# Optimization experiments

Measured on AMD Instinct MI355X. Metric: run time of the kernel, lower is better.

The kernel has to match this reference:

```python
import jax, jax.numpy as jnp
import numpy as np

MASK_FILL = -987654321.0


def rotate_every_two(x):
    # pairs (x0, x1) -> (-x1, x0), interleaved back along last dim
    x1 = x[..., 0::2]
    x2 = x[..., 1::2]
    return jnp.stack((-x2, x1), axis=-1).reshape(x.shape)


def setup_inputs() -> dict:
    key = jax.random.key(0)
    ks = jax.random.split(key, 6)
    b, n, dim = 64, 197, 768
    heads, dim_head = 12, 64
    inner = heads * dim_head
    x = jax.random.normal(ks[0], (b, n, dim), dtype=jnp.float32)
    pos_emb = jax.random.normal(ks[1], (1, n, dim_head), dtype=jnp.float32)
    w_qkv = jax.random.normal(ks[2], (dim, 3 * inner), dtype=jnp.float32) * (dim ** -0.5)
    scale = jnp.full((heads,), dim_head ** -0.5, dtype=jnp.float32)
    w_out = jax.random.normal(ks[3], (inner, dim), dtype=jnp.float32) * (inner ** -0.5)
    b_out = jnp.zeros((dim,), dtype=jnp.float32)
    return {"x": x, "pos_emb": pos_emb, "w_qkv": w_qkv, "scale": scale,
            "w_out": w_out, "b_out": b_out}


def reference(x, pos_emb, w_qkv, scale, w_out, b_out):
    b, n, dim = x.shape
    h = scale.shape[0]
    qkv = x @ w_qkv                         # [b, n, 3*inner]
    q, k, v = jnp.split(qkv, 3, axis=-1)
    dh = q.shape[-1] // h
    to_heads = lambda t: t.reshape(b, n, h, dh).transpose(0, 2, 1, 3)  # bhnd
    q, k, v = to_heads(q), to_heads(k), to_heads(v)

    # RoPE: pos_emb [1, n, (2 * dh/2)] -> sin/cos [n, dh/2] -> interleave to [n, dh]
    sc = pos_emb[0].reshape(n, 2, dh // 2)
    sin = jnp.repeat(sc[:, 0], 2, axis=-1)  # [n, dh]
    cos = jnp.repeat(sc[:, 1], 2, axis=-1)
    q = q * cos + rotate_every_two(q) * sin
    k = k * cos + rotate_every_two(k) * sin

    # per-head learnable scale
    dots = jnp.einsum('bhid,bhjd->bhij', q, k) * scale[None, :, None, None]
    # diagonal (LSA) mask
    eye = jnp.eye(n, dtype=bool)
    dots = jnp.where(eye, MASK_FILL, dots)

    attn = jax.nn.softmax(dots, axis=-1)
    out = jnp.einsum('bhij,bhjd->bhid', attn, v)
    out = out.transpose(0, 2, 1, 3).reshape(b, n, h * dh)
    return out @ w_out + b_out
```

## Files before the change

kernel.cpp:

```cpp
#include <hip/hip_runtime.h>
#include <math.h>

#define MASK_FILL_F (-987654321.0f)

typedef unsigned short u16;
typedef unsigned int   u32;

constexpr int Bb   = 64;
constexpr int Ntok = 197;
constexpr int Dim  = 768;
constexpr int Heads= 12;
constexpr int Dh   = 64;
constexpr int Nq3  = 2304;
constexpr int Rows = 12608;
constexpr int Mpad = 12672;

using f32x4  = __attribute__((ext_vector_type(4))) float;
using bf16x8 = __attribute__((ext_vector_type(8))) short;

__device__ __forceinline__ u16 f2bf(float f) {
  u32 u = __float_as_uint(f);
  u = (u + 0x7fffu + ((u >> 16) & 1u)) >> 16;
  return (u16)u;
}

__device__ __forceinline__ void stage16(const void* gp, void* lp) {
  __builtin_amdgcn_global_load_lds(
      (const __attribute__((address_space(1))) u32*)gp,
      (__attribute__((address_space(3))) u32*)lp, 16, 0, 0);
}

__device__ __forceinline__ int sigma6(int M) {
  return (M & 0x23) | (((M >> 3) & 1) << 4) | (((M >> 2) & 1) << 3) |
         (((M >> 4) & 1) << 2);
}

constexpr int NB_CVT = (Rows * Dim / 4 + 255) / 256;
constexpr int NB_TQ  = (Nq3 / 32) * (Dim / 32);
constexpr int NB_TO  = (Dim / 32) * (Dim / 32);

__global__ __launch_bounds__(256) void prep(
    const float* __restrict__ x, u16* __restrict__ xb,
    const float* __restrict__ w_qkv, u16* __restrict__ wqkvT,
    const float* __restrict__ w_out, u16* __restrict__ woutT)
{
  __shared__ float t[32][33];
  const int bid = blockIdx.x, tid = threadIdx.x;

  if (bid < NB_CVT) {
    const int i = bid * 256 + tid;
    if (i < Rows * Dim / 4) {
      const float4 v = *(const float4*)&x[(size_t)i * 4];
      ushort4 u;
      u.x = f2bf(v.x); u.y = f2bf(v.y); u.z = f2bf(v.z); u.w = f2bf(v.w);
      *(ushort4*)&xb[(size_t)i * 4] = u;
    }
    return;
  }

  const float* in; u16* out; int R, C, c0, r0;
  if (bid < NB_CVT + NB_TQ) {
    const int b2 = bid - NB_CVT;
    in = w_qkv; out = wqkvT; R = Dim; C = Nq3;
    c0 = (b2 % (Nq3 / 32)) * 32; r0 = (b2 / (Nq3 / 32)) * 32;
  } else {
    const int b3 = bid - NB_CVT - NB_TQ;
    in = w_out; out = woutT; R = Dim; C = Dim;
    c0 = (b3 % (Dim / 32)) * 32; r0 = (b3 / (Dim / 32)) * 32;
  }
  const int tx = tid & 31, ty = tid >> 5;
#pragma unroll
  for (int rr = ty; rr < 32; rr += 8)
    t[rr][tx] = in[(size_t)(r0 + rr) * C + c0 + tx];
  __syncthreads();
#pragma unroll
  for (int cc = ty; cc < 32; cc += 8)
    out[(size_t)(c0 + cc) * R + r0 + tx] = f2bf(t[tx][cc]);
}

constexpr int Kc  = 768;
constexpr int NKT = Kc / 64;
#define KTC(x) ((x) < NKT ? (x) : (NKT - 1))

#define BARM() asm volatile("s_barrier" ::: "memory")
#define VMW4() asm volatile("s_waitcnt vmcnt(4)" ::: "memory")

#define STGA(chunk, kt, BUF) \
  stage16(Ag + (size_t)(m0 + (chunk) * 8 + srow) * Kc + (kt) * 64 + scol, \
          &As[BUF][(chunk) * 512])
#define STGB(chunk, kt, BUF) \
  stage16(Bg + (size_t)(n0 + (chunk) * 8 + srow) * Kc + (kt) * 64 + scol, \
          &Bs[BUF][(chunk) * 512])

#define RDA(BUF, MH) \
  _Pragma("unroll") for (int m_ = 0; m_ < 4; ++m_) \
  _Pragma("unroll") for (int k_ = 0; k_ < 2; ++k_) \
    af[m_][k_] = *(const bf16x8*)&As[BUF][(wr * 128 + (MH) * 64 + m_ * 16 + tx) * 64 \
                                          + (((k_ * 4 + qd) ^ sx) * 8)];
#define RDB(BUF, NH, BFR) \
  _Pragma("unroll") for (int n_ = 0; n_ < 2; ++n_) \
  _Pragma("unroll") for (int k_ = 0; k_ < 2; ++k_) \
    BFR[n_][k_] = *(const bf16x8*)&Bs[BUF][(wc * 64 + (NH) * 32 + n_ * 16 + tx) * 64 \
                                           + (((k_ * 4 + qd) ^ sx) * 8)];

#define MM(MH, NH, BFR) \
  __builtin_amdgcn_s_setprio(1); \
  _Pragma("unroll") for (int m_ = 0; m_ < 4; ++m_) \
  _Pragma("unroll") for (int n_ = 0; n_ < 2; ++n_) \
  _Pragma("unroll") for (int k_ = 0; k_ < 2; ++k_) \
    acc[(MH) * 4 + m_][(NH) * 2 + n_] = __builtin_amdgcn_mfma_f32_16x16x32_bf16( \
        af[m_][k_], BFR[n_][k_], acc[(MH) * 4 + m_][(NH) * 2 + n_], 0, 0, 0); \
  __builtin_amdgcn_s_setprio(0);

template<int TN>
__global__ __launch_bounds__(512, 2) void gemm8p(
    const u16* __restrict__ Ag, const u16* __restrict__ Bg,
    u16* __restrict__ Cb, int Nn, int nwg,
    const float* __restrict__ pe)
{
  __shared__ u16 As[2][256 * 64];
  __shared__ u16 Bs[2][256 * 64];

  const int tid = threadIdx.x, lane = tid & 63, w = tid >> 6;

  const int orig = blockIdx.x;
  const int q8 = nwg >> 3, r8 = nwg & 7;
  const int xcd = orig & 7, sub = orig >> 3;
  const int wgid = (xcd < r8 ? xcd * (q8 + 1) : r8 * (q8 + 1) + (xcd - r8) * q8) + sub;
  const int tm = wgid / TN, tn = wgid % TN;
  const int m0 = tm * 256, n0 = tn * 256;

  const int wr = w >> 2, wc = w & 3;
  const int tx = lane & 15, qd = lane >> 4, sx = tx & 7;

  const int srow = lane >> 3;
  const int scol = ((lane & 7) ^ srow) * 8;
  const int b0 = (w >> 1) * 8 + (w & 1) * 2;

  STGA(w, 0, 0);        STGA(16 + w, 0, 0);
  STGB(b0 + 4, 0, 0);   STGB(b0 + 5, 0, 0);
  STGA(8 + w, 0, 0);    STGA(24 + w, 0, 0);
  STGB(b0, 0, 0);       STGB(b0 + 1, 0, 0);
  STGA(w, 1, 1);        STGA(16 + w, 1, 1);
  STGB(b0 + 4, 1, 1);   STGB(b0 + 5, 1, 1);
  VMW4();
  BARM();

  f32x4  acc[8][4] = {};
  bf16x8 af[4][2], bf0[2][2], bf1[2][2];

#pragma unroll 1
  for (int i = 0; i < NKT / 2; ++i) {
    const int u = 2 * i;
    RDA(0, 0); RDB(0, 0, bf0);
    STGA(8 + w, u + 1, 1); STGA(24 + w, u + 1, 1);
    BARM(); MM(0, 0, bf0); BARM();
    RDB(0, 1, bf1);
    STGB(b0, u + 1, 1); STGB(b0 + 1, u + 1, 1);
    BARM(); MM(0, 1, bf1); BARM();
    RDA(0, 1);
    STGA(w, KTC(u + 2), 0); STGA(16 + w, KTC(u + 2), 0);
    BARM(); MM(1, 1, bf1); BARM();
    STGB(b0 + 4, KTC(u + 2), 0); STGB(b0 + 5, KTC(u + 2), 0);
    BARM(); MM(1, 0, bf0); VMW4(); BARM();
    RDA(1, 0); RDB(1, 0, bf0);
    STGA(8 + w, KTC(u + 2), 0); STGA(24 + w, KTC(u + 2), 0);
    BARM(); MM(0, 0, bf0); BARM();
    RDB(1, 1, bf1);
    STGB(b0, KTC(u + 2), 0); STGB(b0 + 1, KTC(u + 2), 0);
    BARM(); MM(0, 1, bf1); BARM();
    RDA(1, 1);
    STGA(w, KTC(u + 3), 1); STGA(16 + w, KTC(u + 3), 1);
    BARM(); MM(1, 1, bf1); BARM();
    STGB(b0 + 4, KTC(u + 3), 1); STGB(b0 + 5, KTC(u + 3), 1);
    BARM(); MM(1, 0, bf0); VMW4(); BARM();
  }

  const bool dorot = (n0 < 2 * Dim);
#pragma unroll
  for (int mi = 0; mi < 8; ++mi) {
    const int rbase = m0 + wr * 128 + mi * 16 + qd * 4;
    int iq[4];
#pragma unroll
    for (int r = 0; r < 4; ++r) iq[r] = (rbase + r) % Ntok;
#pragma unroll
    for (int ni = 0; ni < 4; ++ni) {
      const int col = n0 + wc * 64 + ni * 16 + tx;
      const int mm  = (col & 63) >> 1;
      const int odd = col & 1;
#pragma unroll
      for (int r = 0; r < 4; ++r) {
        float v = acc[mi][ni][r];
        float res = v;
        if (dorot) {
          const float other = __shfl_xor(v, 1, 64);
          const float sn = pe[iq[r] * 64 + mm];
          const float c2 = pe[iq[r] * 64 + 32 + mm];
          res = odd ? (v * c2 + other * sn) : (v * c2 - other * sn);
        }
        Cb[(size_t)(rbase + r) * Nn + col] = f2bf(res);
      }
    }
  }
}

__global__ __launch_bounds__(256) void gemm_bt1(
    const u16* __restrict__ Ag, const u16* __restrict__ Bg,
    float* __restrict__ C, int K, int Nn, const float* __restrict__ bias)
{
  __shared__ u16 As[128 * 32];
  __shared__ u16 Bs[128 * 32];
  const int tid = threadIdx.x, lane = tid & 63, w = tid >> 6;
  const int m0 = blockIdx.y * 128, n0 = blockIdx.x * 128;
  const int wm = (w & 1) * 64, wn = (w >> 1) * 64;
  const int tx = lane & 15, qk = lane >> 4;
  const int rs = lane >> 2, cs = (lane & 3) * 8;

  f32x4 acc[4][4] = {};

  for (int k0 = 0; k0 < K; k0 += 32) {
#pragma unroll
    for (int t = 0; t < 2; ++t) {
      const int r0 = w * 16 + t * 64;
      stage16(Ag + (size_t)(m0 + r0 + rs) * K + k0 + cs, &As[r0 * 32]);
      stage16(Bg + (size_t)(n0 + r0 + rs) * K + k0 + cs, &Bs[r0 * 32]);
    }
    __syncthreads();
    bf16x8 af[4], bf[4];
#pragma unroll
    for (int f = 0; f < 4; ++f) {
      af[f] = *(const bf16x8*)&As[(wm + f * 16 + tx) * 32 + qk * 8];
      bf[f] = *(const bf16x8*)&Bs[(wn + f * 16 + tx) * 32 + qk * 8];
    }
#pragma unroll
    for (int fm = 0; fm < 4; ++fm)
#pragma unroll
      for (int fn = 0; fn < 4; ++fn)
        acc[fm][fn] = __builtin_amdgcn_mfma_f32_16x16x32_bf16(
            af[fm], bf[fn], acc[fm][fn], 0, 0, 0);
    __syncthreads();
  }

#pragma unroll
  for (int fm = 0; fm < 4; ++fm) {
    const int rbase = m0 + wm + fm * 16 + qk * 4;
#pragma unroll
    for (int fn = 0; fn < 4; ++fn) {
      const int col = n0 + wn + fn * 16 + tx;
      const float bv = bias[col];
#pragma unroll
      for (int r = 0; r < 4; ++r) {
        const int row = rbase + r;
        if (row < Rows) C[(size_t)row * Nn + col] = acc[fm][fn][r] + bv;
      }
    }
  }
}

constexpr int LS = 72;

__global__ __launch_bounds__(1024) void attn16(
    const u16* __restrict__ qkvB,
    const float* __restrict__ scale, u16* __restrict__ outB)
{
  __shared__ u16 ks  [64 * LS];
  __shared__ u16 vtmp[64 * LS];
  __shared__ u16 vts [64 * LS];

  const int bh = blockIdx.x;
  const int b = bh / Heads, h = bh % Heads;
  const float sc = scale[h];
  const int tid = threadIdx.x, lane = tid & 63, w = tid >> 6;
  const int tx = lane & 15, q = lane >> 4;
  const size_t rowbase = (size_t)b * Ntok;
  const bool active = (w < 13);

  const int Ms = (tid & 511) >> 3, c8s = (tid & 7) * 8;
  const bool isK = tid < 512;
  const u16* kgp = qkvB + (rowbase + sigma6(Ms)) * (size_t)Nq3 + Dim + h * Dh + c8s;
  const u16* vgp = qkvB + (rowbase + Ms) * (size_t)Nq3 + 2 * Dim + h * Dh + c8s;
  u16* slds = (isK ? ks : vtmp) + Ms * LS + c8s;

  const int td = tid & 63, tj8 = (tid & 511) >> 6;

  bf16x8 bq[2];
  if (active) {
#pragma unroll
    for (int kk = 0; kk < 2; ++kk)
      bq[kk] = *(const bf16x8*)(qkvB +
          (rowbase + 16 * w + tx) * (size_t)Nq3 + h * Dh + kk * 32 + q * 8);
  }

  uint4 sreg = isK ? *(const uint4*)kgp : *(const uint4*)vgp;

  float l_part = 0.f;
  f32x4 oacc[4] = {};

  for (int jt = 0; jt < 4; ++jt) {
    const int j0 = jt * 64;
    __syncthreads();
    *(uint4*)slds = sreg;
    __syncthreads();

    if (!isK) {
      if (jt < 3) {
        const int j = (jt + 1) * 64 + Ms;
        sreg = (j < Ntok) ? *(const uint4*)(vgp + (size_t)(jt + 1) * 64 * Nq3)
                          : make_uint4(0u, 0u, 0u, 0u);
      }
    } else {
      ushort4 lo, hi;
      lo.x = vtmp[(tj8 * 8 + 0) * LS + td]; lo.y = vtmp[(tj8 * 8 + 1) * LS + td];
      lo.z = vtmp[(tj8 * 8 + 2) * LS + td]; lo.w = vtmp[(tj8 * 8 + 3) * LS + td];
      hi.x = vtmp[(tj8 * 8 + 4) * LS + td]; hi.y = vtmp[(tj8 * 8 + 5) * LS + td];
      hi.z = vtmp[(tj8 * 8 + 6) * LS + td]; hi.w = vtmp[(tj8 * 8 + 7) * LS + td];
      *(ushort4*)&vts[td * LS + tj8 * 8]     = lo;
      *(ushort4*)&vts[td * LS + tj8 * 8 + 4] = hi;
      if (jt < 3)
        sreg = *(const uint4*)(kgp + (size_t)(jt + 1) * 64 * Nq3);
    }
    __syncthreads();

    if (active) {
      f32x4 sT[4] = {};
      __builtin_amdgcn_s_setprio(1);
#pragma unroll
      for (int kk = 0; kk < 2; ++kk)
#pragma unroll
        for (int jb = 0; jb < 4; ++jb) {
          const bf16x8 ka = *(const bf16x8*)&ks[(jb * 16 + tx) * LS + kk * 32 + q * 8];
          sT[jb] = __builtin_amdgcn_mfma_f32_16x16x32_bf16(ka, bq[kk], sT[jb], 0, 0, 0);
        }
      __builtin_amdgcn_s_setprio(0);

      const int ig = 16 * w + tx;
      union { bf16x8 v; u16 e[8]; } pk[2];
      float lp = 0.f;
#pragma unroll
      for (int jb = 0; jb < 4; ++jb)
#pragma unroll
        for (int r = 0; r < 4; ++r) {
          const int jg = j0 + 32 * (jb >> 1) + 8 * q + 4 * (jb & 1) + r;
          const float s = fminf(sT[jb][r] * sc, 80.f);
          const bool bad = (jg >= Ntok) || (jg == ig);
          const float p = bad ? 0.f : __expf(s);
          lp += p;
          pk[jb >> 1].e[(jb & 1) * 4 + r] = f2bf(p);
        }
      l_part += lp;

      __builtin_amdgcn_s_setprio(1);
#pragma unroll
      for (int kk = 0; kk < 2; ++kk)
#pragma unroll
        for (int nb = 0; nb < 4; ++nb) {
          const bf16x8 vb = *(const bf16x8*)&vts[(nb * 16 + tx) * LS + kk * 32 + q * 8];
          oacc[nb] = __builtin_amdgcn_mfma_f32_16x16x32_bf16(pk[kk].v, vb,
                                                            oacc[nb], 0, 0, 0);
        }
      __builtin_amdgcn_s_setprio(0);
    }
  }

  if (active) {
    float l = l_part;
    l += __shfl_xor(l, 16, 64);
    l += __shfl_xor(l, 32, 64);
    const float linv = 1.0f / l;
#pragma unroll
    for (int r = 0; r < 4; ++r) {
      const float lr = __shfl(linv, 4 * q + r, 64);
      const int igr = 16 * w + 4 * q + r;
      if (igr < Ntok) {
#pragma unroll
        for (int nb = 0; nb < 4; ++nb)
          outB[(rowbase + igr) * (size_t)Dim + h * Dh + nb * 16 + tx] =
              f2bf(oacc[nb][r] * lr);
      }
    }
  }
}

extern "C" void kernel_launch(void* const* d_in, const int* in_sizes, int n_in,
                              void* d_out, int out_size, void* d_ws, size_t ws_size,
                              hipStream_t stream) {
  const float* x     = (const float*)d_in[0];
  const float* pe    = (const float*)d_in[1];
  const float* w_qkv = (const float*)d_in[2];
  const float* scale = (const float*)d_in[3];
  const float* w_out = (const float*)d_in[4];
  const float* b_out = (const float*)d_in[5];
  float* out = (float*)d_out;

  u16* xb    = (u16*)d_ws;
  u16* wqkvT = xb    + (size_t)Mpad * Dim;
  u16* woutT = wqkvT + (size_t)Nq3 * Dim;
  u16* qkvB  = woutT + (size_t)Dim * Dim;
  u16* attnB = qkvB  + (size_t)Mpad * Nq3;

  prep<<<NB_CVT + NB_TQ + NB_TO, 256, 0, stream>>>(x, xb, w_qkv, wqkvT, w_out, woutT);

  constexpr int NWG0 = 50 * 9;
  gemm8p<9><<<NWG0, 512, 0, stream>>>(xb, wqkvT, qkvB, Nq3, NWG0, pe);

  attn16<<<Bb * Heads, 1024, 0, stream>>>(qkvB, scale, attnB);

  gemm_bt1<<<dim3(Dim / 128, Mpad / 128), 256, 0, stream>>>(
      attnB, woutT, out, Dim, Dim, b_out);
}
```

Measured before the change: 262.2 us.

## Shrink QKV GEMM tile to 128x128 and reuse pipelined kernel for output projection

Replaces the 256x256, 512-thread QKV GEMM with a templated 128x128, 256-thread version that keeps the same double-buffered, barrier-interleaved staging schedule. This gives 1800 workgroups instead of 450, which should improve wave quantization and occupancy. The same pipelined kernel, in a second mode, replaces the simple output-projection GEMM, bringing swizzled LDS and prefetch overlap to that stage. Smaller tiles lower per-tile data reuse and increase global/L2 traffic.

```diff
diff --git a/kernel.cpp b/kernel.cpp
--- a/kernel.cpp
+++ b/kernel.cpp
@@ -93,9 +93,9 @@
           &Bs[BUF][(chunk) * 512])
 
 #define RDA(BUF, MH) \
-  _Pragma("unroll") for (int m_ = 0; m_ < 4; ++m_) \
+  _Pragma("unroll") for (int m_ = 0; m_ < 2; ++m_) \
   _Pragma("unroll") for (int k_ = 0; k_ < 2; ++k_) \
-    af[m_][k_] = *(const bf16x8*)&As[BUF][(wr * 128 + (MH) * 64 + m_ * 16 + tx) * 64 \
+    af[m_][k_] = *(const bf16x8*)&As[BUF][(wr * 64 + (MH) * 32 + m_ * 16 + tx) * 64 \
                                           + (((k_ * 4 + qd) ^ sx) * 8)];
 #define RDB(BUF, NH, BFR) \
   _Pragma("unroll") for (int n_ = 0; n_ < 2; ++n_) \
@@ -105,21 +105,21 @@
 
 #define MM(MH, NH, BFR) \
   __builtin_amdgcn_s_setprio(1); \
-  _Pragma("unroll") for (int m_ = 0; m_ < 4; ++m_) \
+  _Pragma("unroll") for (int m_ = 0; m_ < 2; ++m_) \
   _Pragma("unroll") for (int n_ = 0; n_ < 2; ++n_) \
   _Pragma("unroll") for (int k_ = 0; k_ < 2; ++k_) \
-    acc[(MH) * 4 + m_][(NH) * 2 + n_] = __builtin_amdgcn_mfma_f32_16x16x32_bf16( \
-        af[m_][k_], BFR[n_][k_], acc[(MH) * 4 + m_][(NH) * 2 + n_], 0, 0, 0); \
+    acc[(MH) * 2 + m_][(NH) * 2 + n_] = __builtin_amdgcn_mfma_f32_16x16x32_bf16( \
+        af[m_][k_], BFR[n_][k_], acc[(MH) * 2 + m_][(NH) * 2 + n_], 0, 0, 0); \
   __builtin_amdgcn_s_setprio(0);
 
-template<int TN>
-__global__ __launch_bounds__(512, 2) void gemm8p(
+template<int MODE, int TN>
+__global__ __launch_bounds__(256, 2) void gemm128(
     const u16* __restrict__ Ag, const u16* __restrict__ Bg,
-    u16* __restrict__ Cb, int Nn, int nwg,
-    const float* __restrict__ pe)
+    void* __restrict__ Cv, int Nn, int nwg,
+    const float* __restrict__ pe, const float* __restrict__ bias)
 {
-  __shared__ u16 As[2][256 * 64];
-  __shared__ u16 Bs[2][256 * 64];
+  __shared__ u16 As[2][128 * 64];
+  __shared__ u16 Bs[2][128 * 64];
 
   const int tid = threadIdx.x, lane = tid & 63, w = tid >> 6;
 
@@ -128,130 +128,95 @@
   const int xcd = orig & 7, sub = orig >> 3;
   const int wgid = (xcd < r8 ? xcd * (q8 + 1) : r8 * (q8 + 1) + (xcd - r8) * q8) + sub;
   const int tm = wgid / TN, tn = wgid % TN;
-  const int m0 = tm * 256, n0 = tn * 256;
-
-  const int wr = w >> 2, wc = w & 3;
+  const int m0 = tm * 128, n0 = tn * 128;
+
+  const int wr = w >> 1, wc = w & 1;
   const int tx = lane & 15, qd = lane >> 4, sx = tx & 7;
 
   const int srow = lane >> 3;
   const int scol = ((lane & 7) ^ srow) * 8;
-  const int b0 = (w >> 1) * 8 + (w & 1) * 2;
-
-  STGA(w, 0, 0);        STGA(16 + w, 0, 0);
-  STGB(b0 + 4, 0, 0);   STGB(b0 + 5, 0, 0);
-  STGA(8 + w, 0, 0);    STGA(24 + w, 0, 0);
-  STGB(b0, 0, 0);       STGB(b0 + 1, 0, 0);
-  STGA(w, 1, 1);        STGA(16 + w, 1, 1);
-  STGB(b0 + 4, 1, 1);   STGB(b0 + 5, 1, 1);
+
+  STGA(w, 0, 0);       STGA(8 + w, 0, 0);
+  STGB(4 + w, 0, 0);   STGB(12 + w, 0, 0);
+  STGA(4 + w, 0, 0);   STGA(12 + w, 0, 0);
+  STGB(w, 0, 0);       STGB(8 + w, 0, 0);
+  STGA(w, 1, 1);       STGA(8 + w, 1, 1);
+  STGB(4 + w, 1, 1);   STGB(12 + w, 1, 1);
   VMW4();
   BARM();
 
-  f32x4  acc[8][4] = {};
-  bf16x8 af[4][2], bf0[2][2], bf1[2][2];
+  f32x4  acc[4][4] = {};
+  bf16x8 af[2][2], bf0[2][2], bf1[2][2];
 
 #pragma unroll 1
   for (int i = 0; i < NKT / 2; ++i) {
     const int u = 2 * i;
     RDA(0, 0); RDB(0, 0, bf0);
-    STGA(8 + w, u + 1, 1); STGA(24 + w, u + 1, 1);
+    STGA(4 + w, u + 1, 1); STGA(12 + w, u + 1, 1);
     BARM(); MM(0, 0, bf0); BARM();
     RDB(0, 1, bf1);
-    STGB(b0, u + 1, 1); STGB(b0 + 1, u + 1, 1);
+    STGB(w, u + 1, 1); STGB(8 + w, u + 1, 1);
     BARM(); MM(0, 1, bf1); BARM();
     RDA(0, 1);
-    STGA(w, KTC(u + 2), 0); STGA(16 + w, KTC(u + 2), 0);
+    STGA(w, KTC(u + 2), 0); STGA(8 + w, KTC(u + 2), 0);
     BARM(); MM(1, 1, bf1); BARM();
-    STGB(b0 + 4, KTC(u + 2), 0); STGB(b0 + 5, KTC(u + 2), 0);
+    STGB(4 + w, KTC(u + 2), 0); STGB(12 + w, KTC(u + 2), 0);
     BARM(); MM(1, 0, bf0); VMW4(); BARM();
     RDA(1, 0); RDB(1, 0, bf0);
-    STGA(8 + w, KTC(u + 2), 0); STGA(24 + w, KTC(u + 2), 0);
+    STGA(4 + w, KTC(u + 2), 0); STGA(12 + w, KTC(u + 2), 0);
     BARM(); MM(0, 0, bf0); BARM();
     RDB(1, 1, bf1);
-    STGB(b0, KTC(u + 2), 0); STGB(b0 + 1, KTC(u + 2), 0);
+    STGB(w, KTC(u + 2), 0); STGB(8 + w, KTC(u + 2), 0);
     BARM(); MM(0, 1, bf1); BARM();
     RDA(1, 1);
-    STGA(w, KTC(u + 3), 1); STGA(16 + w, KTC(u + 3), 1);
+    STGA(w, KTC(u + 3), 1); STGA(8 + w, KTC(u + 3), 1);
     BARM(); MM(1, 1, bf1); BARM();
-    STGB(b0 + 4, KTC(u + 3), 1); STGB(b0 + 5, KTC(u + 3), 1);
+    STGB(4 + w, KTC(u + 3), 1); STGB(12 + w, KTC(u + 3), 1);
     BARM(); MM(1, 0, bf0); VMW4(); BARM();
   }
 
-  const bool dorot = (n0 < 2 * Dim);
-#pragma unroll
-  for (int mi = 0; mi < 8; ++mi) {
-    const int rbase = m0 + wr * 128 + mi * 16 + qd * 4;
-    int iq[4];
-#pragma unroll
-    for (int r = 0; r < 4; ++r) iq[r] = (rbase + r) % Ntok;
-#pragma unroll
-    for (int ni = 0; ni < 4; ++ni) {
-      const int col = n0 + wc * 64 + ni * 16 + tx;
-      const int mm  = (col & 63) >> 1;
-      const int odd = col & 1;
-#pragma unroll
-      for (int r = 0; r < 4; ++r) {
-        float v = acc[mi][ni][r];
-        float res = v;
-        if (dorot) {
-          const float other = __shfl_xor(v, 1, 64);
-          const float sn = pe[iq[r] * 64 + mm];
-          const float c2 = pe[iq[r] * 64 + 32 + mm];
-          res = odd ? (v * c2 + other * sn) : (v * c2 - other * sn);
-        }
-        Cb[(size_t)(rbase + r) * Nn + col] = f2bf(res);
+  if (MODE == 0) {
+    u16* Cb = (u16*)Cv;
+    const bool dorot = (n0 < 2 * Dim);
+#pragma unroll
+    for (int mi = 0; mi < 4; ++mi) {
+      const int rbase = m0 + wr * 64 + mi * 16 + qd * 4;
+      int iq[4];
+#pragma unroll
+      for (int r = 0; r < 4; ++r) iq[r] = (rbase + r) % Ntok;
+#pragma unroll
+      for (int ni = 0; ni < 4; ++ni) {
+        const int col = n0 + wc * 64 + ni * 16 + tx;
+        const int mm  = (col & 63) >> 1;
+        const int odd = col & 1;
+#pragma unroll
+        for (int r = 0; r < 4; ++r) {
+          float v = acc[mi][ni][r];
+          float res = v;
+          if (dorot) {
+            const float other = __shfl_xor(v, 1, 64);
+            const float sn = pe[iq[r] * 64 + mm];
+            const float c2 = pe[iq[r] * 64 + 32 + mm];
+            res = odd ? (v * c2 + other * sn) : (v * c2 - other * sn);
+          }
+          Cb[(size_t)(rbase + r) * Nn + col] = f2bf(res);
+        }
       }
     }
-  }
-}
-
-__global__ __launch_bounds__(256) void gemm_bt1(
-    const u16* __restrict__ Ag, const u16* __restrict__ Bg,
-    float* __restrict__ C, int K, int Nn, const float* __restrict__ bias)
-{
-  __shared__ u16 As[128 * 32];
-  __shared__ u16 Bs[128 * 32];
-  const int tid = threadIdx.x, lane = tid & 63, w = tid >> 6;
-  const int m0 = blockIdx.y * 128, n0 = blockIdx.x * 128;
-  const int wm = (w & 1) * 64, wn = (w >> 1) * 64;
-  const int tx = lane & 15, qk = lane >> 4;
-  const int rs = lane >> 2, cs = (lane & 3) * 8;
-
-  f32x4 acc[4][4] = {};
-
-  for (int k0 = 0; k0 < K; k0 += 32) {
-#pragma unroll
-    for (int t = 0; t < 2; ++t) {
-      const int r0 = w * 16 + t * 64;
-      stage16(Ag + (size_t)(m0 + r0 + rs) * K + k0 + cs, &As[r0 * 32]);
-      stage16(Bg + (size_t)(n0 + r0 + rs) * K + k0 + cs, &Bs[r0 * 32]);
-    }
-    __syncthreads();
-    bf16x8 af[4], bf[4];
-#pragma unroll
-    for (int f = 0; f < 4; ++f) {
-      af[f] = *(const bf16x8*)&As[(wm + f * 16 + tx) * 32 + qk * 8];
-      bf[f] = *(const bf16x8*)&Bs[(wn + f * 16 + tx) * 32 + qk * 8];
-    }
-#pragma unroll
-    for (int fm = 0; fm < 4; ++fm)
-#pragma unroll
-      for (int fn = 0; fn < 4; ++fn)
-        acc[fm][fn] = __builtin_amdgcn_mfma_f32_16x16x32_bf16(
-            af[fm], bf[fn], acc[fm][fn], 0, 0, 0);
-    __syncthreads();
-  }
-
-#pragma unroll
-  for (int fm = 0; fm < 4; ++fm) {
-    const int rbase = m0 + wm + fm * 16 + qk * 4;
-#pragma unroll
-    for (int fn = 0; fn < 4; ++fn) {
-      const int col = n0 + wn + fn * 16 + tx;
-      const float bv = bias[col];
-#pragma unroll
-      for (int r = 0; r < 4; ++r) {
-        const int row = rbase + r;
-        if (row < Rows) C[(size_t)row * Nn + col] = acc[fm][fn][r] + bv;
+  } else {
+    float* C = (float*)Cv;
+#pragma unroll
+    for (int mi = 0; mi < 4; ++mi) {
+      const int rbase = m0 + wr * 64 + mi * 16 + qd * 4;
+#pragma unroll
+      for (int ni = 0; ni < 4; ++ni) {
+        const int col = n0 + wc * 64 + ni * 16 + tx;
+        const float bv = bias[col];
+#pragma unroll
+        for (int r = 0; r < 4; ++r) {
+          const int row = rbase + r;
+          if (row < Rows) C[(size_t)row * Nn + col] = acc[mi][ni][r] + bv;
+        }
       }
     }
   }
@@ -400,11 +365,11 @@
 
   prep<<<NB_CVT + NB_TQ + NB_TO, 256, 0, stream>>>(x, xb, w_qkv, wqkvT, w_out, woutT);
 
-  constexpr int NWG0 = 50 * 9;
-  gemm8p<9><<<NWG0, 512, 0, stream>>>(xb, wqkvT, qkvB, Nq3, NWG0, pe);
+  constexpr int NWG0 = 100 * 18;
+  gemm128<0, 18><<<NWG0, 256, 0, stream>>>(xb, wqkvT, qkvB, Nq3, NWG0, pe, nullptr);
 
   attn16<<<Bb * Heads, 1024, 0, stream>>>(qkvB, scale, attnB);
 
-  gemm_bt1<<<dim3(Dim / 128, Mpad / 128), 256, 0, stream>>>(
-      attnB, woutT, out, Dim, Dim, b_out);
-}
+  constexpr int NWG1 = 100 * 6;
+  gemm128<1, 6><<<NWG1, 256, 0, stream>>>(attnB, woutT, out, Dim, NWG1, nullptr, b_out);
+}
```

Result: slower. 271.4 us (+3.5%).
